# Kernel tuning notes

Hardware: AMD Instinct MI355X
Metric: run time of the kernel (lower is better)

Reference implementation:

```python
import jax, jax.numpy as jnp
import numpy as np
from jax import lax

N, HW = 64, 240
C0, C1, C2, C3 = 3, 32, 64, 128
HEAD = 1280


def _conv(x, w, stride, pad):
    return lax.conv_general_dilated(
        x, w, (stride, stride), [(pad, pad), (pad, pad)],
        dimension_numbers=("NCHW", "OIHW", "NCHW"))


def _cbr(x, w, alpha, beta, stride, pad, do_relu=True):
    # conv2d with pre-folded BN: y = conv(x,w)*alpha + beta, then ReLU
    y = _conv(x, w, stride, pad)
    y = y * alpha[None, :, None, None] + beta[None, :, None, None]
    return jnp.maximum(y, 0.0) if do_relu else y


def setup_inputs() -> dict:
    key = jax.random.key(0)
    ks = jax.random.split(key, 13)
    f32 = jnp.float32
    inp = {
        "x": jax.random.normal(ks[0], (N, C0, HW, HW), dtype=f32),
        # stem 3x3 s2: 3 -> 32
        "w_stem": jax.random.normal(ks[1], (C1, C0, 3, 3), dtype=f32) * 0.1,
        "a_stem": jax.random.uniform(ks[2], (C1,), dtype=f32, minval=0.5, maxval=1.5),
        "b_stem": jax.random.normal(ks[3], (C1,), dtype=f32) * 0.1,
        # mid 3x3 s2: 32 -> 64
        "w1": jax.random.normal(ks[4], (C2, C1, 3, 3), dtype=f32) * 0.05,
        "a1": jax.random.uniform(ks[5], (C2,), dtype=f32, minval=0.5, maxval=1.5),
        "b1": jax.random.normal(ks[6], (C2,), dtype=f32) * 0.1,
        # pointwise 1x1 s1: 64 -> 128
        "w2": jax.random.normal(ks[7], (C3, C2, 1, 1), dtype=f32) * 0.05,
        "a2": jax.random.uniform(ks[8], (C3,), dtype=f32, minval=0.5, maxval=1.5),
        "b2": jax.random.normal(ks[9], (C3,), dtype=f32) * 0.1,
        # head: GAP + GEMV (w2d [Cout, Cin]) + BN-fold + ReLU
        "w_head": jax.random.normal(ks[10], (HEAD, C3), dtype=f32) * 0.05,
        "a_head": jax.random.uniform(ks[11], (HEAD,), dtype=f32, minval=0.5, maxval=1.5),
        "b_head": jax.random.normal(ks[12], (HEAD,), dtype=f32) * 0.1,
    }
    return inp


def reference(x, w_stem, a_stem, b_stem, w1, a1, b1, w2, a2, b2,
              w_head, a_head, b_head):
    h = _cbr(x, w_stem, a_stem, b_stem, stride=2, pad=1)   # [N,32,120,120]
    h = _cbr(h, w1, a1, b1, stride=2, pad=1)               # [N,64,60,60]
    h = _cbr(h, w2, a2, b2, stride=1, pad=0)               # [N,128,60,60]
    # head: global average pool + GEMV + folded-BN affine + ReLU
    gap = h.mean(axis=(2, 3))                              # [N,128]
    out = jnp.einsum("nc,oc->no", gap, w_head)             # [N,1280]
    out = out * a_head[None, :] + b_head[None, :]
    return jnp.maximum(out, 0.0)
```

## Files before the change

kernel.cpp:

```cpp
#include <hip/hip_runtime.h>

#define N_    64
#define HW_   240
#define H1_   120
#define H2_   60
#define C0_   3
#define C1_   32
#define C2_   64
#define C3_   128
#define HEAD_ 1280

typedef unsigned short US;
typedef short bf16x8 __attribute__((ext_vector_type(8)));
typedef float f32x16 __attribute__((ext_vector_type(16)));

__device__ __forceinline__ US f2bf(float f) {
  union { float f; unsigned u; } v; v.f = f;
  unsigned r = v.u + 0x7FFF + ((v.u >> 16) & 1);
  return (US)(r >> 16);
}

#define H1Q_ROW 3968
#define H1Q_PL  1984

#define ZCHN   368
#define ZTOT   (64 * ZCHN * 4)
__global__ __launch_bounds__(256) void k0_prep(
    const float* __restrict__ w1, const float* __restrict__ w2,
    const float* __restrict__ w0,
    US* __restrict__ h1q, US* __restrict__ wt1, US* __restrict__ wt2,
    US* __restrict__ wt0, float* __restrict__ gap) {
  int gid = blockIdx.x * 256 + threadIdx.x;
  if (gid < ZTOT) {
    int c = gid >> 2, q = gid & 3;
    int n = c / ZCHN, cc = c % ZCHN;
    long off; int y;
    if (cc < 124)      { y = 0;   off = (long)cc * 32; }
    else if (cc < 248) { y = 121; off = (long)(cc - 124) * 32; }
    else               { y = cc - 247; off = H1Q_PL; }
    uint4 z; z.x = z.y = z.z = z.w = 0u;
    *(uint4*)(h1q + ((long)(n * 122 + y)) * H1Q_ROW + off + q * 8) = z;
  } else if (gid < ZTOT + 18432) {
    int e = gid - ZTOT;
    int oc = e / 288, ic = (e / 9) % 32, ky = (e / 3) % 3, kx = e % 3;
    wt1[((ky * 3 + kx) * 64 + oc) * 32 + ic] = f2bf(w1[e]);
  } else if (gid < ZTOT + 18432 + 8192) {
    int e = gid - (ZTOT + 18432);
    wt2[e] = f2bf(w2[e]);
  } else if (gid < ZTOT + 18432 + 8192 + 1024) {
    int e = gid - (ZTOT + 18432 + 8192);
    int oc = e >> 5, k = e & 31;
    wt0[e] = (k < 27) ? f2bf(w0[oc * 27 + k]) : (US)0;
  } else if (gid < ZTOT + 18432 + 8192 + 1024 + 8192) {
    gap[gid - (ZTOT + 18432 + 8192 + 1024)] = 0.f;
  }
}

#define XSW 248
__global__ __launch_bounds__(256) void k1_mfma(
    const float* __restrict__ x, const US* __restrict__ wt0,
    const float* __restrict__ alpha, const float* __restrict__ beta,
    US* __restrict__ h1q) {
  __shared__ float xs[3 * 3 * XSW];
  __shared__ US ot[128 * 32];
  int y = blockIdx.x, n = blockIdx.y;
  int iy0 = 2 * y - 1;
  const float* xn = x + (long)n * C0_ * HW_ * HW_;
  for (int e = threadIdx.x; e < 540; e += 256) {
    int m = e % 60, seg = e / 60;
    int ic = seg / 3, r = seg % 3;
    int iy = iy0 + r;
    float4 v; v.x = v.y = v.z = v.w = 0.f;
    if (iy >= 0) v = *(const float4*)(xn + (long)ic * HW_ * HW_ + iy * HW_ + 4 * m);
    *(float4*)(xs + seg * XSW + 4 + 4 * m) = v;
  }
  if (threadIdx.x < 18) {
    int seg = threadIdx.x >> 1, end = threadIdx.x & 1;
    float4 z; z.x = z.y = z.z = z.w = 0.f;
    *(float4*)(xs + seg * XSW + (end ? 244 : 0)) = z;
  }
  __syncthreads();

  int t = threadIdx.x, wv = t >> 6, l = t & 63;
  int lane31 = l & 31, half = l >> 5;
  int ox = wv * 32 + lane31;
  int oxc = ox < H1_ ? ox : (H1_ - 1);

  float fa[16];
#pragma unroll
  for (int m = 0; m < 2; m++)
#pragma unroll
    for (int j = 0; j < 8; j++) {
      int k = m * 16 + half * 8 + j;
      float v = 0.f;
      if (k < 27) {
        int ic = k / 9, rem = k - ic * 9;
        int ky = rem / 3, kx = rem - ky * 3;
        v = xs[(ic * 3 + ky) * XSW + 3 + 2 * oxc + kx];
      }
      fa[m * 8 + j] = v;
    }
  bf16x8 a0, a1;
#pragma unroll
  for (int j = 0; j < 8; j++) {
    a0[j] = (short)f2bf(fa[j]);
    a1[j] = (short)f2bf(fa[8 + j]);
  }
  const US* wb = wt0 + lane31 * 32 + half * 8;
  bf16x8 b0 = *(const bf16x8*)(wb);
  bf16x8 b1 = *(const bf16x8*)(wb + 16);

  f32x16 acc;
#pragma unroll
  for (int i = 0; i < 16; i++) acc[i] = 0.f;
  acc = __builtin_amdgcn_mfma_f32_32x32x16_bf16(a0, b0, acc, 0, 0, 0);
  acc = __builtin_amdgcn_mfma_f32_32x32x16_bf16(a1, b1, acc, 0, 0, 0);

  int oc = lane31;
  float al = alpha[oc], be = beta[oc];
#pragma unroll
  for (int r = 0; r < 16; r++) {
    int row = (r & 3) + 8 * (r >> 2) + 4 * half;
    float v = fmaxf(fmaf(acc[r], al, be), 0.f);
    ot[(wv * 32 + row) * 32 + oc] = f2bf(v);
  }
  __syncthreads();

  long rowb = ((long)(n * 122 + y + 1)) * H1Q_ROW;
  for (int u = t; u < 480; u += 256) {
    int px = u >> 2, q = u & 3;
    int pl = px & 1;
    int m = (px + 1) >> 1;
    long addr = rowb + (pl ? H1Q_PL : 0) + (long)m * 32 + q * 8;
    *(uint4*)(h1q + addr) = *(const uint4*)(ot + px * 32 + q * 8);
  }
}

#define TS 72
__global__ __launch_bounds__(256) void k2_fused(
    const US* __restrict__ h1q, const US* __restrict__ wt1,
    const US* __restrict__ wt2,
    const float* __restrict__ a1, const float* __restrict__ b1,
    const float* __restrict__ a2, const float* __restrict__ b2,
    float* __restrict__ gap) {
  __shared__ US tile[128 * TS];
  int n = blockIdx.y, tileb = blockIdx.x;
  int t = threadIdx.x, w = t >> 6, l = t & 63;
  int wm = w & 1, wn = w >> 1;
  int lane31 = l & 31, half = l >> 5;
  int oc = wn * 32 + lane31;

  int pxb0 = tileb * 128 + wm * 64;
  int pxb1 = pxb0 + 32;
  int p0 = pxb0 + lane31; int pc0 = p0 < 3600 ? p0 : 3599;
  int p1 = pxb1 + lane31; int pc1 = p1 < 3600 ? p1 : 3599;
  int y0 = pc0 / 60, xx0 = pc0 % 60;
  int y1 = pc1 / 60, xx1 = pc1 % 60;

  f32x16 accA, accB;
#pragma unroll
  for (int i = 0; i < 16; i++) { accA[i] = 0.f; accB[i] = 0.f; }

#pragma unroll
  for (int ky = 0; ky < 3; ky++) {
    const US* c0a1 = h1q + ((long)(n * 122 + 2 * y0 + ky)) * H1Q_ROW
                         + (long)xx0 * 32 + half * 8;
    const US* c1a1 = h1q + ((long)(n * 122 + 2 * y1 + ky)) * H1Q_ROW
                         + (long)xx1 * 32 + half * 8;
    const US* wk = wt1 + (ky * 3) * (64 * 32) + oc * 32 + half * 8;
#pragma unroll
    for (int kx = 0; kx < 3; kx++) {
      long aoff = (kx == 1) ? 0 : (kx == 0 ? H1Q_PL : (H1Q_PL + 32));
      const US* bp = wk + kx * (64 * 32);
#pragma unroll
      for (int c = 0; c < 2; c++) {
        bf16x8 bv  = *(const bf16x8*)(bp + c * 16);
        bf16x8 av0 = *(const bf16x8*)(c0a1 + aoff + c * 16);
        bf16x8 av1 = *(const bf16x8*)(c1a1 + aoff + c * 16);
        accA = __builtin_amdgcn_mfma_f32_32x32x16_bf16(av0, bv, accA, 0, 0, 0);
        accB = __builtin_amdgcn_mfma_f32_32x32x16_bf16(av1, bv, accB, 0, 0, 0);
      }
    }
  }
  {
    float al = a1[oc], be = b1[oc];
#pragma unroll
    for (int r = 0; r < 16; r++) {
      int row = (r & 3) + 8 * (r >> 2) + 4 * half;
      float vA = fmaxf(fmaf(accA[r], al, be), 0.f);
      float vB = fmaxf(fmaf(accB[r], al, be), 0.f);
      tile[(wm * 64 + row) * TS + oc] = f2bf(vA);
      tile[(wm * 64 + 32 + row) * TS + oc] = f2bf(vB);
    }
  }
  __syncthreads();

  int base_px = tileb * 128 + w * 32;
  const US* abase2 = tile + (w * 32 + lane31) * TS + half * 8;
  bf16x8 af[4];
#pragma unroll
  for (int c = 0; c < 4; c++) af[c] = *(const bf16x8*)(abase2 + c * 16);

#pragma unroll
  for (int nt = 0; nt < 4; nt++) {
    int oc2 = nt * 32 + lane31;
    const US* bb = wt2 + oc2 * 64 + half * 8;
    f32x16 acc2;
#pragma unroll
    for (int i = 0; i < 16; i++) acc2[i] = 0.f;
#pragma unroll
    for (int c = 0; c < 4; c++) {
      bf16x8 bv = *(const bf16x8*)(bb + c * 16);
      acc2 = __builtin_amdgcn_mfma_f32_32x32x16_bf16(af[c], bv, acc2, 0, 0, 0);
    }
    float al2 = a2[oc2], be2 = b2[oc2];
    float s = 0.f;
    if (base_px + 31 < 3600) {
#pragma unroll
      for (int r = 0; r < 16; r++) s += fmaxf(fmaf(acc2[r], al2, be2), 0.f);
    } else {
#pragma unroll
      for (int r = 0; r < 16; r++) {
        int row = (r & 3) + 8 * (r >> 2) + 4 * half;
        if (base_px + row < 3600) s += fmaxf(fmaf(acc2[r], al2, be2), 0.f);
      }
    }
    s += __shfl_xor(s, 32);
    if (half == 0) atomicAdd(gap + n * C3_ + oc2, s);
  }
}

__global__ __launch_bounds__(256) void k4_head(
    const float* __restrict__ gap, const float* __restrict__ wh,
    const float* __restrict__ alpha, const float* __restrict__ beta,
    float* __restrict__ out) {
  __shared__ float g[C3_];
  int n = blockIdx.y;
  int o = blockIdx.x * 256 + threadIdx.x;
  if (threadIdx.x < C3_)
    g[threadIdx.x] = gap[n * C3_ + threadIdx.x] * (1.f / 3600.f);
  __syncthreads();
  const float* wr = wh + (long)o * C3_;
  float acc = 0.f;
#pragma unroll 8
  for (int c = 0; c < C3_; c += 4) {
    float4 wv = *(const float4*)(wr + c);
    acc = fmaf(wv.x, g[c],     acc);
    acc = fmaf(wv.y, g[c + 1], acc);
    acc = fmaf(wv.z, g[c + 2], acc);
    acc = fmaf(wv.w, g[c + 3], acc);
  }
  out[n * HEAD_ + o] = fmaxf(fmaf(acc, alpha[o], beta[o]), 0.f);
}

extern "C" void kernel_launch(void* const* d_in, const int* in_sizes, int n_in,
                              void* d_out, int out_size, void* d_ws,
                              size_t ws_size, hipStream_t stream) {
  const float* x      = (const float*)d_in[0];
  const float* w_stem = (const float*)d_in[1];
  const float* a_stem = (const float*)d_in[2];
  const float* b_stem = (const float*)d_in[3];
  const float* w1     = (const float*)d_in[4];
  const float* a1     = (const float*)d_in[5];
  const float* b1     = (const float*)d_in[6];
  const float* w2     = (const float*)d_in[7];
  const float* a2     = (const float*)d_in[8];
  const float* b2     = (const float*)d_in[9];
  const float* wh     = (const float*)d_in[10];
  const float* ah     = (const float*)d_in[11];
  const float* bh     = (const float*)d_in[12];
  float* out = (float*)d_out;

  US* h1q = (US*)d_ws;
  US* wt1 = h1q + (size_t)N_ * 122 * H1Q_ROW;
  US* wt2 = wt1 + 9 * 64 * 32;
  US* wt0 = wt2 + C3_ * C2_;
  float* gap = (float*)(wt0 + 1024);

  {
    int total = ZTOT + 18432 + 8192 + 1024 + 8192;
    k0_prep<<<(total + 255) / 256, 256, 0, stream>>>(w1, w2, w_stem, h1q,
                                                     wt1, wt2, wt0, gap);
  }
  {
    dim3 grid(H1_, N_);
    k1_mfma<<<grid, 256, 0, stream>>>(x, wt0, a_stem, b_stem, h1q);
  }
  {
    dim3 grid(29, N_);
    k2_fused<<<grid, 256, 0, stream>>>(h1q, wt1, wt2, a1, b1, a2, b2, gap);
  }
  {
    dim3 grid(HEAD_ / 256, N_);
    k4_head<<<grid, 256, 0, stream>>>(gap, wh, ah, bh, out);
  }
}
```

Measured before the change: 172.5 us.

## Restructure k2 to one output row per block with LDS-staged swizzled input

The fused conv2+pointwise kernel now processes one 60-pixel output row per block instead of 128 flattened pixels. The three needed input rows are staged into LDS with direct global-to-LDS loads and an XOR swizzle to avoid bank conflicts. The block order is remapped for locality. This removes redundant per-lane global loads of overlapping input rows. In exchange there are more blocks (60 vs 29 per image), about 6% padding waste on the 64-row tile, and the 1x1 stage is split across waves by output-channel group.

```diff
diff --git a/kernel.cpp b/kernel.cpp
--- a/kernel.cpp
+++ b/kernel.cpp
@@ -137,48 +137,59 @@
 }
 
 #define TS 72
+__device__ __forceinline__ void gld_lds16(const void* g, void* l) {
+  __builtin_amdgcn_global_load_lds(
+      (const __attribute__((address_space(1))) unsigned int*)g,
+      (__attribute__((address_space(3))) unsigned int*)l, 16, 0, 0);
+}
+
 __global__ __launch_bounds__(256) void k2_fused(
     const US* __restrict__ h1q, const US* __restrict__ wt1,
     const US* __restrict__ wt2,
     const float* __restrict__ a1, const float* __restrict__ b1,
     const float* __restrict__ a2, const float* __restrict__ b2,
     float* __restrict__ gap) {
-  __shared__ US tile[128 * TS];
-  int n = blockIdx.y, tileb = blockIdx.x;
+  __shared__ __align__(16) US st[1536 * 8];
+  __shared__ __align__(16) US tile[64 * TS];
   int t = threadIdx.x, w = t >> 6, l = t & 63;
+  int lane31 = l & 31, half = l >> 5;
+
+  int flat = blockIdx.y * 60 + blockIdx.x;
+  int sf = (flat & 7) * 480 + (flat >> 3);
+  int n = sf / 60, y = sf - n * 60;
+
+  const US* src = h1q + ((long)(n * 122 + 2 * y)) * H1Q_ROW;
+#pragma unroll
+  for (int i = 0; i < 6; i++) {
+    int b = (i * 256 + t) * 16;
+    int sb = b ^ (((b >> 7) & 7) << 4);
+    gld_lds16((const char*)src + sb, (char*)st + b);
+  }
+  __syncthreads();
+
   int wm = w & 1, wn = w >> 1;
-  int lane31 = l & 31, half = l >> 5;
+  int px = wm * 32 + lane31;
+  int xx = px < 60 ? px : 59;
   int oc = wn * 32 + lane31;
-
-  int pxb0 = tileb * 128 + wm * 64;
-  int pxb1 = pxb0 + 32;
-  int p0 = pxb0 + lane31; int pc0 = p0 < 3600 ? p0 : 3599;
-  int p1 = pxb1 + lane31; int pc1 = p1 < 3600 ? p1 : 3599;
-  int y0 = pc0 / 60, xx0 = pc0 % 60;
-  int y1 = pc1 / 60, xx1 = pc1 % 60;
-
-  f32x16 accA, accB;
-#pragma unroll
-  for (int i = 0; i < 16; i++) { accA[i] = 0.f; accB[i] = 0.f; }
+  int abase = xx * 32 + half * 8;
+
+  f32x16 acc;
+#pragma unroll
+  for (int i = 0; i < 16; i++) acc[i] = 0.f;
 
 #pragma unroll
   for (int ky = 0; ky < 3; ky++) {
-    const US* c0a1 = h1q + ((long)(n * 122 + 2 * y0 + ky)) * H1Q_ROW
-                         + (long)xx0 * 32 + half * 8;
-    const US* c1a1 = h1q + ((long)(n * 122 + 2 * y1 + ky)) * H1Q_ROW
-                         + (long)xx1 * 32 + half * 8;
-    const US* wk = wt1 + (ky * 3) * (64 * 32) + oc * 32 + half * 8;
 #pragma unroll
     for (int kx = 0; kx < 3; kx++) {
-      long aoff = (kx == 1) ? 0 : (kx == 0 ? H1Q_PL : (H1Q_PL + 32));
-      const US* bp = wk + kx * (64 * 32);
+      int aoff = ky * 3968 + (kx == 1 ? 0 : (kx == 0 ? 1984 : 2016)) + abase;
+      const US* wk = wt1 + ((ky * 3 + kx) * 64 + oc) * 32 + half * 8;
 #pragma unroll
       for (int c = 0; c < 2; c++) {
-        bf16x8 bv  = *(const bf16x8*)(bp + c * 16);
-        bf16x8 av0 = *(const bf16x8*)(c0a1 + aoff + c * 16);
-        bf16x8 av1 = *(const bf16x8*)(c1a1 + aoff + c * 16);
-        accA = __builtin_amdgcn_mfma_f32_32x32x16_bf16(av0, bv, accA, 0, 0, 0);
-        accB = __builtin_amdgcn_mfma_f32_32x32x16_bf16(av1, bv, accB, 0, 0, 0);
+        int u = aoff + c * 16;
+        int us = u ^ (((u >> 6) & 7) << 3);
+        bf16x8 av = *(const bf16x8*)(st + us);
+        bf16x8 bv = *(const bf16x8*)(wk + c * 16);
+        acc = __builtin_amdgcn_mfma_f32_32x32x16_bf16(av, bv, acc, 0, 0, 0);
       }
     }
   }
@@ -187,23 +198,21 @@
 #pragma unroll
     for (int r = 0; r < 16; r++) {
       int row = (r & 3) + 8 * (r >> 2) + 4 * half;
-      float vA = fmaxf(fmaf(accA[r], al, be), 0.f);
-      float vB = fmaxf(fmaf(accB[r], al, be), 0.f);
-      tile[(wm * 64 + row) * TS + oc] = f2bf(vA);
-      tile[(wm * 64 + 32 + row) * TS + oc] = f2bf(vB);
-    }
-  }
-  __syncthreads();
-
-  int base_px = tileb * 128 + w * 32;
-  const US* abase2 = tile + (w * 32 + lane31) * TS + half * 8;
+      tile[(wm * 32 + row) * TS + oc] = f2bf(fmaxf(fmaf(acc[r], al, be), 0.f));
+    }
+  }
+  __syncthreads();
+
+  int pt = w & 1;
+  int og = w >> 1;
+  const US* ab = tile + (pt * 32 + lane31) * TS + half * 8;
   bf16x8 af[4];
 #pragma unroll
-  for (int c = 0; c < 4; c++) af[c] = *(const bf16x8*)(abase2 + c * 16);
-
-#pragma unroll
-  for (int nt = 0; nt < 4; nt++) {
-    int oc2 = nt * 32 + lane31;
+  for (int c = 0; c < 4; c++) af[c] = *(const bf16x8*)(ab + c * 16);
+
+#pragma unroll
+  for (int nt = 0; nt < 2; nt++) {
+    int oc2 = (og * 2 + nt) * 32 + lane31;
     const US* bb = wt2 + oc2 * 64 + half * 8;
     f32x16 acc2;
 #pragma unroll
@@ -215,14 +224,14 @@
     }
     float al2 = a2[oc2], be2 = b2[oc2];
     float s = 0.f;
-    if (base_px + 31 < 3600) {
+    if (pt == 0) {
 #pragma unroll
       for (int r = 0; r < 16; r++) s += fmaxf(fmaf(acc2[r], al2, be2), 0.f);
     } else {
 #pragma unroll
       for (int r = 0; r < 16; r++) {
         int row = (r & 3) + 8 * (r >> 2) + 4 * half;
-        if (base_px + row < 3600) s += fmaxf(fmaf(acc2[r], al2, be2), 0.f);
+        if (32 + row < 60) s += fmaxf(fmaf(acc2[r], al2, be2), 0.f);
       }
     }
     s += __shfl_xor(s, 32);
@@ -287,7 +296,7 @@
     k1_mfma<<<grid, 256, 0, stream>>>(x, wt0, a_stem, b_stem, h1q);
   }
   {
-    dim3 grid(29, N_);
+    dim3 grid(H2_, N_);
     k2_fused<<<grid, 256, 0, stream>>>(h1q, wt1, wt2, a1, b1, a2, b2, gap);
   }
   {
```

Result: no change. 169.2 us (-1.9%).
